# Kernel tuning notes

Measured on AMD Instinct MI355X. Metric: run time of the kernel, lower is better.

The kernel has to match this reference:

```python
import jax, jax.numpy as jnp
import numpy as np

MIN_MZ, MAX_MZ, BIN_W = 0.0, 1000.0, 0.01
NUM_BINS = int((MAX_MZ - MIN_MZ) / BIN_W)      # 100000
GROUP, OUT_PER_GROUP = 30, 3
GROUPS = NUM_BINS // GROUP                      # 3333
BINNER_OUT = GROUPS * OUT_PER_GROUP             # 9999
SCALING = 0.5
EPS = 1e-6
B, P = 256, 512                                 # pairs, padded peaks per spectrum


def setup_inputs() -> dict:
    key = jax.random.key(0)
    ks = jax.random.split(key, 10)
    # mz drawn in [0, 1100): peaks >= max_mz are dropped by the range filter (ragged-like)
    mz = jax.random.uniform(ks[0], (B, 2, P), jnp.float32, 0.0, 1100.0)
    intensities = jax.random.uniform(ks[1], (B, 2, P), jnp.float32, 1e-3, 1.0)
    s = 0.02
    return dict(
        mz=mz,
        intensities=intensities,
        binner_w=jax.random.normal(ks[2], (GROUPS, GROUP, OUT_PER_GROUP), jnp.float32) * s,
        binner_b=jax.random.normal(ks[3], (GROUPS, OUT_PER_GROUP), jnp.float32) * s,
        w0=jax.random.normal(ks[4], (BINNER_OUT, 1000), jnp.float32) * s,
        b0=jnp.zeros((1000,), jnp.float32),
        w1=jax.random.normal(ks[5], (1000, 800), jnp.float32) * s,
        b1=jnp.zeros((800,), jnp.float32),
        w2=jax.random.normal(ks[6], (800, 800), jnp.float32) * s,
        b2=jnp.zeros((800,), jnp.float32),
        we=jax.random.normal(ks[7], (800, 400), jnp.float32) * s,
        be=jnp.zeros((400,), jnp.float32),
    )


def _bin_spectra(mz, inten):
    # mz, inten: [N, P] -> binned [N, NUM_BINS] via ragged scatter-add of inten**SCALING
    mzc = jax.lax.stop_gradient(mz)             # indices are non-differentiable
    mask = (mzc >= MIN_MZ) & (mzc < MAX_MZ)
    idx = jnp.clip(((mzc - MIN_MZ) / BIN_W).astype(jnp.int32), 0, NUM_BINS - 1)
    vals = jnp.where(mask, inten ** SCALING, 0.0)
    n = mz.shape[0]
    rows = jnp.arange(n)[:, None]               # [N,1] broadcast against [N,P]
    binned = jnp.zeros((n, NUM_BINS), jnp.float32)
    return binned.at[rows, idx].add(vals)


def _encoder(binned, binner_w, binner_b, w0, b0, w1, b1, w2, b2, we, be):
    n = binned.shape[0]
    # PeakBinner: block-diagonal micro-linears over groups of 30 bins (last 10 bins unused)
    xg = binned[:, : GROUPS * GROUP].reshape(n, GROUPS, GROUP)
    x = jnp.einsum('bgi,gio->bgo', xg, binner_w) + binner_b
    x = x.reshape(n, BINNER_OUT)
    x = jax.nn.relu(x @ w0 + b0)
    x = jax.nn.relu(x @ w1 + b1)                # dropout = identity at eval
    x = jax.nn.relu(x @ w2 + b2)
    return x @ we + be                           # [N, 400]


def reference(mz, intensities, binner_w, binner_b, w0, b0, w1, b1, w2, b2, we, be):
    bp = mz.shape[0]
    n = bp * 2
    binned = _bin_spectra(mz.reshape(n, P), intensities.reshape(n, P))
    emb = _encoder(binned, binner_w, binner_b, w0, b0, w1, b1, w2, b2, we, be)
    emb = emb.reshape(bp, 2, -1)
    e1, e2 = emb[:, 0], emb[:, 1]
    n1 = jnp.maximum(jnp.linalg.norm(e1, axis=1), EPS)
    n2 = jnp.maximum(jnp.linalg.norm(e2, axis=1), EPS)
    return jnp.sum(e1 * e2, axis=1) / (n1 * n2)  # [B] cosine similarity
```

## Files before the change

### kernel.cpp

```cpp
#include <hip/hip_runtime.h>

typedef __bf16 bf16;
typedef __bf16 bf16x8 __attribute__((ext_vector_type(8)));
typedef float  f32x4  __attribute__((ext_vector_type(4)));

#define NSPEC   512
#define BOUT    9999
#define K0A     10240
#define N00     1024
#define N01     896
#define N02     896
#define N03     448

__device__ __forceinline__ void gload_lds16(const bf16* g, bf16* l) {
    auto* gp = reinterpret_cast<const __attribute__((address_space(1))) unsigned int*>(
        reinterpret_cast<uintptr_t>(g));
    auto* lp = reinterpret_cast<__attribute__((address_space(3))) unsigned int*>(
        reinterpret_cast<uintptr_t>(l));
    __builtin_amdgcn_global_load_lds(gp, lp, 16, 0, 0);
}

__device__ __forceinline__ void transpose_tile64(const float* __restrict__ src,
                                                 bf16* __restrict__ dst,
                                                 int K, int N, int K0,
                                                 float* tile, int bx, int by) {
    int n0 = bx * 64, k0 = by * 32;
    int t = threadIdx.x;
    {
        int kr = t >> 4, nc = (t & 15) * 4;
        int gk = k0 + kr;
#pragma unroll
        for (int e = 0; e < 4; ++e) {
            int gn = n0 + nc + e;
            tile[kr * 65 + nc + e] = (gk < K && gn < N) ? src[(size_t)gk * N + gn] : 0.0f;
        }
    }
    __syncthreads();
    {
        int nr = t >> 3, kc = (t & 7) * 4;
        bf16 v[4];
#pragma unroll
        for (int e = 0; e < 4; ++e) v[e] = (bf16)tile[(kc + e) * 65 + nr];
        *(ushort4*)&dst[(size_t)(n0 + nr) * K0 + k0 + kc] = *(ushort4*)v;
    }
}

__global__ __launch_bounds__(512) void prep_all(const float* __restrict__ mz,
                                                const float* __restrict__ inten,
                                                const float* __restrict__ bw,
                                                const float* __restrict__ bb,
                                                const float* __restrict__ w0,
                                                const float* __restrict__ w1,
                                                const float* __restrict__ w2,
                                                const float* __restrict__ we,
                                                bf16* __restrict__ A,
                                                bf16* __restrict__ B0t,
                                                bf16* __restrict__ B1t,
                                                bf16* __restrict__ B2t,
                                                bf16* __restrict__ BEt,
                                                float* __restrict__ psums) {
    __shared__ float smem[K0A];
    int b = blockIdx.x;
    if (b < 5120) {
        transpose_tile64(w0, B0t, BOUT, 1000, K0A, smem, b & 15, b >> 4);
    } else if (b < 5568) {
        int r = b - 5120;
        transpose_tile64(w1, B1t, 1000, 800, 1024, smem, r % 14, r / 14);
    } else if (b < 5960) {
        int r = b - 5568;
        transpose_tile64(w2, B2t, 800, 800, 896, smem, r % 14, r / 14);
    } else if (b < 6156) {
        int r = b - 5960;
        transpose_tile64(we, BEt, 800, 400, 896, smem, r % 7, r / 7);
    } else if (b < 6668) {
        const int spec = b - 6156;
        const int t = threadIdx.x;
#pragma unroll
        for (int i = 0; i < 5; ++i)
            *(float4*)&smem[(i * 512 + t) * 4] = float4{0.f, 0.f, 0.f, 0.f};
        __syncthreads();
        {
            float m = mz[(size_t)spec * 512 + t];
            float v = inten[(size_t)spec * 512 + t];
            bool mask = (m >= 0.0f) && (m < 1000.0f);
            int idx = (int)(m / 0.01f);
            idx = min(max(idx, 0), 99999);
            if (mask && idx < 99990) {
                int g = idx / 30;
                float val = sqrtf(v);
                const float* w = bw + (size_t)idx * 3;
                atomicAdd(&smem[g * 3 + 0], val * w[0]);
                atomicAdd(&smem[g * 3 + 1], val * w[1]);
                atomicAdd(&smem[g * 3 + 2], val * w[2]);
            }
        }
        __syncthreads();
        bf16* Arow = A + (size_t)spec * K0A;
#pragma unroll
        for (int i = 0; i < 5; ++i) {
            int c = (i * 512 + t) * 4;
            float4 s = *(const float4*)&smem[c];
            bf16 o[4];
            o[0] = (bf16)((c + 0 < BOUT) ? bb[c + 0] + s.x : 0.f);
            o[1] = (bf16)((c + 1 < BOUT) ? bb[c + 1] + s.y : 0.f);
            o[2] = (bf16)((c + 2 < BOUT) ? bb[c + 2] + s.z : 0.f);
            o[3] = (bf16)((c + 3 < BOUT) ? bb[c + 3] + s.w : 0.f);
            *(ushort4*)&Arow[c] = *(ushort4*)o;
        }
    } else {
        for (int i = threadIdx.x; i < 768; i += 512) psums[i] = 0.f;
    }
}

__global__ __launch_bounds__(256) void gemm0_splitk(const bf16* __restrict__ A,
                                                    const bf16* __restrict__ Bt,
                                                    float* __restrict__ Cslab) {
    constexpr int K0 = K0A, KITERS = 20, BK = 64;
    __shared__ __align__(16) bf16 As[2][64 * BK];
    __shared__ __align__(16) bf16 Bs[2][64 * BK];
    const int bid = blockIdx.x;
    const int kp = bid & 7;
    const int tile = bid >> 3;
    const int mt = tile & 7, nt = tile >> 3;
    const int tid = threadIdx.x, wave = tid >> 6, lane = tid & 63;
    const int wm = wave & 1, wn = wave >> 1;
    const int lrow = lane & 15, quad = lane >> 4;

    const bf16* Ag = A  + (size_t)(mt * 64) * K0 + kp * KITERS * BK;
    const bf16* Bg = Bt + (size_t)(nt * 64) * K0 + kp * KITERS * BK;

    auto stage = [&](int buf, int kk) {
        const int k = kk * BK;
#pragma unroll
        for (int j = 0; j < 2; ++j) {
            int row0 = j * 32 + wave * 8;
            int row = row0 + (lane >> 3);
            int ch  = (lane & 7) ^ (row & 7);
            gload_lds16(Ag + (size_t)row * K0 + k + ch * 8, &As[buf][row0 * BK]);
            gload_lds16(Bg + (size_t)row * K0 + k + ch * 8, &Bs[buf][row0 * BK]);
        }
    };

    f32x4 acc[2][2] = {};
    stage(0, 0);
    for (int kk = 0; kk < KITERS; ++kk) {
        const int cur = kk & 1;
        __syncthreads();
        if (kk + 1 < KITERS) stage(cur ^ 1, kk + 1);
#pragma unroll
        for (int ks = 0; ks < 2; ++ks) {
            bf16x8 af[2], bfr[2];
#pragma unroll
            for (int im = 0; im < 2; ++im) {
                int r = wm * 32 + im * 16 + lrow;
                int c = ks * 4 + quad;
                af[im] = *(const bf16x8*)&As[cur][r * BK + ((c ^ (r & 7)) << 3)];
            }
#pragma unroll
            for (int in = 0; in < 2; ++in) {
                int r = wn * 32 + in * 16 + lrow;
                int c = ks * 4 + quad;
                bfr[in] = *(const bf16x8*)&Bs[cur][r * BK + ((c ^ (r & 7)) << 3)];
            }
#pragma unroll
            for (int im = 0; im < 2; ++im)
#pragma unroll
                for (int in = 0; in < 2; ++in)
                    acc[im][in] = __builtin_amdgcn_mfma_f32_16x16x32_bf16(af[im], bfr[in], acc[im][in], 0, 0, 0);
        }
    }
    float* C = Cslab + (size_t)kp * (NSPEC * N00);
#pragma unroll
    for (int im = 0; im < 2; ++im) {
        int row0 = mt * 64 + wm * 32 + im * 16 + quad * 4;
#pragma unroll
        for (int in = 0; in < 2; ++in) {
            int col = nt * 64 + wn * 32 + in * 16 + lrow;
#pragma unroll
            for (int r = 0; r < 4; ++r)
                C[(size_t)(row0 + r) * N00 + col] = acc[im][in][r];
        }
    }
}

__global__ __launch_bounds__(256) void reduce_bias_relu(const float* __restrict__ Cslab,
                                                        const float* __restrict__ b0,
                                                        bf16* __restrict__ H0b) {
    int idx = blockIdx.x * 256 + threadIdx.x;
    int r = idx >> 8, c = (idx & 255) * 4;
    float4 s = {0.f, 0.f, 0.f, 0.f};
#pragma unroll
    for (int kp = 0; kp < 8; ++kp) {
        float4 v = *(const float4*)&Cslab[(size_t)kp * (NSPEC * N00) + (size_t)r * N00 + c];
        s.x += v.x; s.y += v.y; s.z += v.z; s.w += v.w;
    }
    bf16 o[4];
    o[0] = (bf16)fmaxf(s.x + ((c + 0 < 1000) ? b0[c + 0] : 0.f), 0.f);
    o[1] = (bf16)fmaxf(s.y + ((c + 1 < 1000) ? b0[c + 1] : 0.f), 0.f);
    o[2] = (bf16)fmaxf(s.z + ((c + 2 < 1000) ? b0[c + 2] : 0.f), 0.f);
    o[3] = (bf16)fmaxf(s.w + ((c + 3 < 1000) ? b0[c + 3] : 0.f), 0.f);
    *(ushort4*)&H0b[(size_t)r * N00 + c] = *(ushort4*)o;
}

__global__ __launch_bounds__(256) void gemm_small(const bf16* __restrict__ A,
                                                  const bf16* __restrict__ Bt,
                                                  const float* __restrict__ bias,
                                                  bf16* __restrict__ Ob,
                                                  int K0, int N0, int Nreal,
                                                  int kiters, int ntiles) {
    __shared__ __align__(16) bf16 As[2][32 * 128];
    __shared__ __align__(16) bf16 Bs[2][32 * 128];
    const int bid = blockIdx.x;
    const int mt = bid / ntiles, nt = bid % ntiles;
    const int tid = threadIdx.x, wave = tid >> 6, lane = tid & 63;
    const int wm = wave & 1, wn = wave >> 1;
    const int lrow = lane & 15, quad = lane >> 4;

    const bf16* Ag = A  + (size_t)(mt * 32) * K0;
    const bf16* Bg = Bt + (size_t)(nt * 32) * K0;

    auto stage = [&](int buf, int kk) {
        const int k = kk * 128;
#pragma unroll
        for (int j = wave; j < 8; j += 4) {
            int row0 = j * 4;
            int row = row0 + (lane >> 4);
            int ch  = (lane & 15) ^ (row & 15);
            gload_lds16(Ag + (size_t)row * K0 + k + ch * 8, &As[buf][row0 * 128]);
            gload_lds16(Bg + (size_t)row * K0 + k + ch * 8, &Bs[buf][row0 * 128]);
        }
    };

    f32x4 acc = {};
    stage(0, 0);
    for (int kk = 0; kk < kiters; ++kk) {
        const int cur = kk & 1;
        __syncthreads();
        if (kk + 1 < kiters) stage(cur ^ 1, kk + 1);
#pragma unroll
        for (int ks = 0; ks < 4; ++ks) {
            int ra = wm * 16 + lrow, rb = wn * 16 + lrow;
            int c = ks * 4 + quad;
            bf16x8 af  = *(const bf16x8*)&As[cur][ra * 128 + ((c ^ (ra & 15)) << 3)];
            bf16x8 bfr = *(const bf16x8*)&Bs[cur][rb * 128 + ((c ^ (rb & 15)) << 3)];
            acc = __builtin_amdgcn_mfma_f32_16x16x32_bf16(af, bfr, acc, 0, 0, 0);
        }
    }
    int row0 = mt * 32 + wm * 16 + quad * 4;
    int col  = nt * 32 + wn * 16 + lrow;
    float bv = (col < Nreal) ? bias[col] : 0.f;
#pragma unroll
    for (int r = 0; r < 4; ++r) {
        float v = fmaxf(acc[r] + bv, 0.f);
        Ob[(size_t)(row0 + r) * N0 + col] = (bf16)v;
    }
}

__global__ __launch_bounds__(256) void gemm_last(const bf16* __restrict__ A,
                                                 const bf16* __restrict__ Bt,
                                                 const float* __restrict__ bias,
                                                 float* __restrict__ psums,
                                                 int K0, int kiters, int ntiles) {
    __shared__ __align__(16) bf16 As[2][32 * 128];
    __shared__ __align__(16) bf16 Bs[2][32 * 128];
    const int bid = blockIdx.x;
    const int mt = bid / ntiles, nt = bid % ntiles;
    const int tid = threadIdx.x, wave = tid >> 6, lane = tid & 63;
    const int wm = wave & 1, wn = wave >> 1;
    const int lrow = lane & 15, quad = lane >> 4;

    const bf16* Ag = A  + (size_t)(mt * 32) * K0;
    const bf16* Bg = Bt + (size_t)(nt * 32) * K0;

    auto stage = [&](int buf, int kk) {
        const int k = kk * 128;
#pragma unroll
        for (int j = wave; j < 8; j += 4) {
            int row0 = j * 4;
            int row = row0 + (lane >> 4);
            int ch  = (lane & 15) ^ (row & 15);
            gload_lds16(Ag + (size_t)row * K0 + k + ch * 8, &As[buf][row0 * 128]);
            gload_lds16(Bg + (size_t)row * K0 + k + ch * 8, &Bs[buf][row0 * 128]);
        }
    };

    f32x4 acc = {};
    stage(0, 0);
    for (int kk = 0; kk < kiters; ++kk) {
        const int cur = kk & 1;
        __syncthreads();
        if (kk + 1 < kiters) stage(cur ^ 1, kk + 1);
#pragma unroll
        for (int ks = 0; ks < 4; ++ks) {
            int ra = wm * 16 + lrow, rb = wn * 16 + lrow;
            int c = ks * 4 + quad;
            bf16x8 af  = *(const bf16x8*)&As[cur][ra * 128 + ((c ^ (ra & 15)) << 3)];
            bf16x8 bfr = *(const bf16x8*)&Bs[cur][rb * 128 + ((c ^ (rb & 15)) << 3)];
            acc = __builtin_amdgcn_mfma_f32_16x16x32_bf16(af, bfr, acc, 0, 0, 0);
        }
    }
    int rowbase = mt * 32 + wm * 16 + quad * 4;
    int col     = nt * 32 + wn * 16 + lrow;
    bool valid  = (col < 400);
    float bv = valid ? bias[col] : 0.f;
    float v[4];
#pragma unroll
    for (int r = 0; r < 4; ++r) v[r] = valid ? (acc[r] + bv) : 0.f;
    int p0 = rowbase >> 1;
    float sums[6] = {v[0] * v[1], v[0] * v[0], v[1] * v[1],
                     v[2] * v[3], v[2] * v[2], v[3] * v[3]};
#pragma unroll
    for (int off = 1; off < 16; off <<= 1)
#pragma unroll
        for (int s = 0; s < 6; ++s) sums[s] += __shfl_xor(sums[s], off);
    if (lrow == 0) {
#pragma unroll
        for (int s = 0; s < 3; ++s) {
            atomicAdd(&psums[(p0 + 0) * 3 + s], sums[s]);
            atomicAdd(&psums[(p0 + 1) * 3 + s], sums[3 + s]);
        }
    }
}

__global__ __launch_bounds__(256) void cosine_fin(const float* __restrict__ psums,
                                                  float* __restrict__ out) {
    int t = threadIdx.x;
    float d  = psums[t * 3 + 0];
    float s1 = psums[t * 3 + 1];
    float s2 = psums[t * 3 + 2];
    float n1 = fmaxf(sqrtf(s1), 1e-6f);
    float n2 = fmaxf(sqrtf(s2), 1e-6f);
    out[t] = d / (n1 * n2);
}

extern "C" void kernel_launch(void* const* d_in, const int* in_sizes, int n_in,
                              void* d_out, int out_size, void* d_ws, size_t ws_size,
                              hipStream_t stream) {
    const float* mz    = (const float*)d_in[0];
    const float* inten = (const float*)d_in[1];
    const float* bw    = (const float*)d_in[2];
    const float* bb    = (const float*)d_in[3];
    const float* w0    = (const float*)d_in[4];
    const float* b0    = (const float*)d_in[5];
    const float* w1    = (const float*)d_in[6];
    const float* b1    = (const float*)d_in[7];
    const float* w2    = (const float*)d_in[8];
    const float* b2    = (const float*)d_in[9];
    const float* we    = (const float*)d_in[10];
    const float* be    = (const float*)d_in[11];
    float* out = (float*)d_out;

    char* ws = (char*)d_ws;
    size_t off = 0;
    auto alloc = [&](size_t bytes) { char* p = ws + off; off += (bytes + 255) & ~(size_t)255; return p; };
    bf16*  A     = (bf16*) alloc((size_t)NSPEC * K0A * 2);
    bf16*  B0t   = (bf16*) alloc((size_t)N00 * K0A * 2);
    bf16*  B1t   = (bf16*) alloc((size_t)N01 * 1024 * 2);
    bf16*  B2t   = (bf16*) alloc((size_t)N02 * 896 * 2);
    bf16*  BEt   = (bf16*) alloc((size_t)N03 * 896 * 2);
    float* Cslab = (float*)alloc((size_t)8 * NSPEC * N00 * 4);
    bf16*  H0b   = (bf16*) alloc((size_t)NSPEC * N00 * 2);
    bf16*  H1b   = (bf16*) alloc((size_t)NSPEC * N01 * 2);
    bf16*  H2b   = (bf16*) alloc((size_t)NSPEC * N02 * 2);
    float* psums = (float*)alloc(768 * 4);

    prep_all<<<6669, 512, 0, stream>>>(mz, inten, bw, bb, w0, w1, w2, we,
                                       A, B0t, B1t, B2t, BEt, psums);
    gemm0_splitk<<<1024, 256, 0, stream>>>(A, B0t, Cslab);
    reduce_bias_relu<<<512, 256, 0, stream>>>(Cslab, b0, H0b);
    gemm_small<<<448, 256, 0, stream>>>(H0b, B1t, b1, H1b, 1024, N01, 800, 8, 28);
    gemm_small<<<448, 256, 0, stream>>>(H1b, B2t, b2, H2b, 896,  N02, 800, 7, 28);
    gemm_last<<<224, 256, 0, stream>>>(H2b, BEt, be, psums, 896, 7, 14);
    cosine_fin<<<1, 256, 0, stream>>>(psums, out);
}
```

Baseline: 167.5 us.

## Double gemm0 split-K with bf16 partials and intra-block split-K tail GEMMs

The first GEMM's split-K factor goes from 8 to 16 and its partial slabs are stored in bf16 instead of fp32, so more blocks run and the slab traffic into the reduction shrinks. The three tail GEMMs become one templated 512-thread kernel with BK=256. Two wave groups each take half of every K tile and their accumulators are combined through LDS. To support this, the tail weights and activations are padded to K=1024 and the pad columns are zeroed in prep. Rounding partial sums to bf16 adds error before they are accumulated.

```diff
diff --git a/kernel.cpp b/kernel.cpp
--- a/kernel.cpp
+++ b/kernel.cpp
@@ -8,9 +8,7 @@
 #define BOUT    9999
 #define K0A     10240
 #define N00     1024
-#define N01     896
-#define N02     896
-#define N03     448
+#define KSPLIT0 16
 
 __device__ __forceinline__ void gload_lds16(const bf16* g, bf16* l) {
     auto* gp = reinterpret_cast<const __attribute__((address_space(1))) unsigned int*>(
@@ -58,6 +56,8 @@
                                                 bf16* __restrict__ B1t,
                                                 bf16* __restrict__ B2t,
                                                 bf16* __restrict__ BEt,
+                                                bf16* __restrict__ H1b,
+                                                bf16* __restrict__ H2b,
                                                 float* __restrict__ psums) {
     __shared__ float smem[K0A];
     int b = blockIdx.x;
@@ -66,14 +66,14 @@
     } else if (b < 5568) {
         int r = b - 5120;
         transpose_tile64(w1, B1t, 1000, 800, 1024, smem, r % 14, r / 14);
-    } else if (b < 5960) {
+    } else if (b < 6016) {
         int r = b - 5568;
-        transpose_tile64(w2, B2t, 800, 800, 896, smem, r % 14, r / 14);
-    } else if (b < 6156) {
-        int r = b - 5960;
-        transpose_tile64(we, BEt, 800, 400, 896, smem, r % 7, r / 7);
-    } else if (b < 6668) {
-        const int spec = b - 6156;
+        transpose_tile64(w2, B2t, 800, 800, 1024, smem, r % 14, r / 14);
+    } else if (b < 6240) {
+        int r = b - 6016;
+        transpose_tile64(we, BEt, 800, 400, 1024, smem, r % 7, r / 7);
+    } else if (b < 6752) {
+        const int spec = b - 6240;
         const int t = threadIdx.x;
 #pragma unroll
         for (int i = 0; i < 5; ++i)
@@ -107,6 +107,14 @@
             o[3] = (bf16)((c + 3 < BOUT) ? bb[c + 3] + s.w : 0.f);
             *(ushort4*)&Arow[c] = *(ushort4*)o;
         }
+    } else if (b < 6784) {
+        int idx = b - 6752;
+        bf16* H = (idx < 16) ? H1b : H2b;
+        int sub = idx & 15;
+        int t = threadIdx.x;
+        int row = sub * 32 + (t >> 4);
+        int col = 896 + (t & 15) * 8;
+        *(uint4*)&H[(size_t)row * 1024 + col] = uint4{0u, 0u, 0u, 0u};
     } else {
         for (int i = threadIdx.x; i < 768; i += 512) psums[i] = 0.f;
     }
@@ -114,20 +122,20 @@
 
 __global__ __launch_bounds__(256) void gemm0_splitk(const bf16* __restrict__ A,
                                                     const bf16* __restrict__ Bt,
-                                                    float* __restrict__ Cslab) {
-    constexpr int K0 = K0A, KITERS = 20, BK = 64;
+                                                    bf16* __restrict__ Cslab) {
+    constexpr int K0 = K0A, KITERS = 10, BK = 64;
     __shared__ __align__(16) bf16 As[2][64 * BK];
     __shared__ __align__(16) bf16 Bs[2][64 * BK];
     const int bid = blockIdx.x;
-    const int kp = bid & 7;
-    const int tile = bid >> 3;
+    const int kp = bid & 15;
+    const int tile = bid >> 4;
     const int mt = tile & 7, nt = tile >> 3;
     const int tid = threadIdx.x, wave = tid >> 6, lane = tid & 63;
     const int wm = wave & 1, wn = wave >> 1;
     const int lrow = lane & 15, quad = lane >> 4;
 
-    const bf16* Ag = A  + (size_t)(mt * 64) * K0 + kp * KITERS * BK;
-    const bf16* Bg = Bt + (size_t)(nt * 64) * K0 + kp * KITERS * BK;
+    const bf16* Ag = A  + (size_t)(mt * 64) * K0 + kp * (KITERS * BK);
+    const bf16* Bg = Bt + (size_t)(nt * 64) * K0 + kp * (KITERS * BK);
 
     auto stage = [&](int buf, int kk) {
         const int k = kk * BK;
@@ -169,7 +177,7 @@
                     acc[im][in] = __builtin_amdgcn_mfma_f32_16x16x32_bf16(af[im], bfr[in], acc[im][in], 0, 0, 0);
         }
     }
-    float* C = Cslab + (size_t)kp * (NSPEC * N00);
+    bf16* C = Cslab + (size_t)kp * (NSPEC * N00);
 #pragma unroll
     for (int im = 0; im < 2; ++im) {
         int row0 = mt * 64 + wm * 32 + im * 16 + quad * 4;
@@ -178,146 +186,111 @@
             int col = nt * 64 + wn * 32 + in * 16 + lrow;
 #pragma unroll
             for (int r = 0; r < 4; ++r)
-                C[(size_t)(row0 + r) * N00 + col] = acc[im][in][r];
-        }
-    }
-}
-
-__global__ __launch_bounds__(256) void reduce_bias_relu(const float* __restrict__ Cslab,
+                C[(size_t)(row0 + r) * N00 + col] = (bf16)acc[im][in][r];
+        }
+    }
+}
+
+__global__ __launch_bounds__(256) void reduce_bias_relu(const bf16* __restrict__ Cslab,
                                                         const float* __restrict__ b0,
                                                         bf16* __restrict__ H0b) {
     int idx = blockIdx.x * 256 + threadIdx.x;
-    int r = idx >> 8, c = (idx & 255) * 4;
-    float4 s = {0.f, 0.f, 0.f, 0.f};
-#pragma unroll
-    for (int kp = 0; kp < 8; ++kp) {
-        float4 v = *(const float4*)&Cslab[(size_t)kp * (NSPEC * N00) + (size_t)r * N00 + c];
-        s.x += v.x; s.y += v.y; s.z += v.z; s.w += v.w;
-    }
-    bf16 o[4];
-    o[0] = (bf16)fmaxf(s.x + ((c + 0 < 1000) ? b0[c + 0] : 0.f), 0.f);
-    o[1] = (bf16)fmaxf(s.y + ((c + 1 < 1000) ? b0[c + 1] : 0.f), 0.f);
-    o[2] = (bf16)fmaxf(s.z + ((c + 2 < 1000) ? b0[c + 2] : 0.f), 0.f);
-    o[3] = (bf16)fmaxf(s.w + ((c + 3 < 1000) ? b0[c + 3] : 0.f), 0.f);
-    *(ushort4*)&H0b[(size_t)r * N00 + c] = *(ushort4*)o;
-}
-
-__global__ __launch_bounds__(256) void gemm_small(const bf16* __restrict__ A,
-                                                  const bf16* __restrict__ Bt,
-                                                  const float* __restrict__ bias,
-                                                  bf16* __restrict__ Ob,
-                                                  int K0, int N0, int Nreal,
-                                                  int kiters, int ntiles) {
-    __shared__ __align__(16) bf16 As[2][32 * 128];
-    __shared__ __align__(16) bf16 Bs[2][32 * 128];
+    int r = idx >> 7, c = (idx & 127) * 8;
+    float s[8] = {};
+#pragma unroll
+    for (int kp = 0; kp < KSPLIT0; ++kp) {
+        bf16x8 v = *(const bf16x8*)&Cslab[(size_t)kp * (NSPEC * N00) + (size_t)r * N00 + c];
+#pragma unroll
+        for (int j = 0; j < 8; ++j) s[j] += (float)v[j];
+    }
+    bf16 o[8];
+#pragma unroll
+    for (int j = 0; j < 8; ++j)
+        o[j] = (bf16)fmaxf(s[j] + ((c + j < 1000) ? b0[c + j] : 0.f), 0.f);
+    *(uint4*)&H0b[(size_t)r * N00 + c] = *(uint4*)o;
+}
+
+template <bool LAST>
+__global__ __launch_bounds__(512) void gemm_tail(const bf16* __restrict__ A,
+                                                 const bf16* __restrict__ Bt,
+                                                 const float* __restrict__ bias,
+                                                 bf16* __restrict__ Ob,
+                                                 float* __restrict__ psums,
+                                                 int Nreal, int ntiles) {
+    constexpr int BK = 256, KITERS = 4;
+    __shared__ __align__(16) bf16 As[2][32 * BK];
+    __shared__ __align__(16) bf16 Bs[2][32 * BK];
+    __shared__ f32x4 xacc[4][64];
     const int bid = blockIdx.x;
     const int mt = bid / ntiles, nt = bid % ntiles;
     const int tid = threadIdx.x, wave = tid >> 6, lane = tid & 63;
-    const int wm = wave & 1, wn = wave >> 1;
+    const int g = wave >> 2, w2 = wave & 3;
+    const int wm = w2 & 1, wn = w2 >> 1;
     const int lrow = lane & 15, quad = lane >> 4;
 
-    const bf16* Ag = A  + (size_t)(mt * 32) * K0;
-    const bf16* Bg = Bt + (size_t)(nt * 32) * K0;
+    const bf16* Ag = A  + (size_t)(mt * 32) * 1024;
+    const bf16* Bg = Bt + (size_t)(nt * 32) * 1024;
 
     auto stage = [&](int buf, int kk) {
-        const int k = kk * 128;
-#pragma unroll
-        for (int j = wave; j < 8; j += 4) {
-            int row0 = j * 4;
-            int row = row0 + (lane >> 4);
-            int ch  = (lane & 15) ^ (row & 15);
-            gload_lds16(Ag + (size_t)row * K0 + k + ch * 8, &As[buf][row0 * 128]);
-            gload_lds16(Bg + (size_t)row * K0 + k + ch * 8, &Bs[buf][row0 * 128]);
+        const int k = kk * BK;
+#pragma unroll
+        for (int j = 0; j < 2; ++j) {
+            int row0 = (wave + j * 8) * 2;
+            int row = row0 + (lane >> 5);
+            int ch  = (lane & 31) ^ (row & 31);
+            gload_lds16(Ag + (size_t)row * 1024 + k + ch * 8, &As[buf][row0 * BK]);
+            gload_lds16(Bg + (size_t)row * 1024 + k + ch * 8, &Bs[buf][row0 * BK]);
         }
     };
 
     f32x4 acc = {};
     stage(0, 0);
-    for (int kk = 0; kk < kiters; ++kk) {
+    for (int kk = 0; kk < KITERS; ++kk) {
         const int cur = kk & 1;
         __syncthreads();
-        if (kk + 1 < kiters) stage(cur ^ 1, kk + 1);
+        if (kk + 1 < KITERS) stage(cur ^ 1, kk + 1);
 #pragma unroll
         for (int ks = 0; ks < 4; ++ks) {
             int ra = wm * 16 + lrow, rb = wn * 16 + lrow;
-            int c = ks * 4 + quad;
-            bf16x8 af  = *(const bf16x8*)&As[cur][ra * 128 + ((c ^ (ra & 15)) << 3)];
-            bf16x8 bfr = *(const bf16x8*)&Bs[cur][rb * 128 + ((c ^ (rb & 15)) << 3)];
+            int c = g * 16 + ks * 4 + quad;
+            bf16x8 af  = *(const bf16x8*)&As[cur][ra * BK + ((c ^ (ra & 31)) << 3)];
+            bf16x8 bfr = *(const bf16x8*)&Bs[cur][rb * BK + ((c ^ (rb & 31)) << 3)];
             acc = __builtin_amdgcn_mfma_f32_16x16x32_bf16(af, bfr, acc, 0, 0, 0);
         }
     }
-    int row0 = mt * 32 + wm * 16 + quad * 4;
-    int col  = nt * 32 + wn * 16 + lrow;
-    float bv = (col < Nreal) ? bias[col] : 0.f;
-#pragma unroll
-    for (int r = 0; r < 4; ++r) {
-        float v = fmaxf(acc[r] + bv, 0.f);
-        Ob[(size_t)(row0 + r) * N0 + col] = (bf16)v;
-    }
-}
-
-__global__ __launch_bounds__(256) void gemm_last(const bf16* __restrict__ A,
-                                                 const bf16* __restrict__ Bt,
-                                                 const float* __restrict__ bias,
-                                                 float* __restrict__ psums,
-                                                 int K0, int kiters, int ntiles) {
-    __shared__ __align__(16) bf16 As[2][32 * 128];
-    __shared__ __align__(16) bf16 Bs[2][32 * 128];
-    const int bid = blockIdx.x;
-    const int mt = bid / ntiles, nt = bid % ntiles;
-    const int tid = threadIdx.x, wave = tid >> 6, lane = tid & 63;
-    const int wm = wave & 1, wn = wave >> 1;
-    const int lrow = lane & 15, quad = lane >> 4;
-
-    const bf16* Ag = A  + (size_t)(mt * 32) * K0;
-    const bf16* Bg = Bt + (size_t)(nt * 32) * K0;
-
-    auto stage = [&](int buf, int kk) {
-        const int k = kk * 128;
-#pragma unroll
-        for (int j = wave; j < 8; j += 4) {
-            int row0 = j * 4;
-            int row = row0 + (lane >> 4);
-            int ch  = (lane & 15) ^ (row & 15);
-            gload_lds16(Ag + (size_t)row * K0 + k + ch * 8, &As[buf][row0 * 128]);
-            gload_lds16(Bg + (size_t)row * K0 + k + ch * 8, &Bs[buf][row0 * 128]);
-        }
-    };
-
-    f32x4 acc = {};
-    stage(0, 0);
-    for (int kk = 0; kk < kiters; ++kk) {
-        const int cur = kk & 1;
-        __syncthreads();
-        if (kk + 1 < kiters) stage(cur ^ 1, kk + 1);
-#pragma unroll
-        for (int ks = 0; ks < 4; ++ks) {
-            int ra = wm * 16 + lrow, rb = wn * 16 + lrow;
-            int c = ks * 4 + quad;
-            bf16x8 af  = *(const bf16x8*)&As[cur][ra * 128 + ((c ^ (ra & 15)) << 3)];
-            bf16x8 bfr = *(const bf16x8*)&Bs[cur][rb * 128 + ((c ^ (rb & 15)) << 3)];
-            acc = __builtin_amdgcn_mfma_f32_16x16x32_bf16(af, bfr, acc, 0, 0, 0);
-        }
-    }
-    int rowbase = mt * 32 + wm * 16 + quad * 4;
-    int col     = nt * 32 + wn * 16 + lrow;
-    bool valid  = (col < 400);
-    float bv = valid ? bias[col] : 0.f;
-    float v[4];
-#pragma unroll
-    for (int r = 0; r < 4; ++r) v[r] = valid ? (acc[r] + bv) : 0.f;
-    int p0 = rowbase >> 1;
-    float sums[6] = {v[0] * v[1], v[0] * v[0], v[1] * v[1],
-                     v[2] * v[3], v[2] * v[2], v[3] * v[3]};
-#pragma unroll
-    for (int off = 1; off < 16; off <<= 1)
-#pragma unroll
-        for (int s = 0; s < 6; ++s) sums[s] += __shfl_xor(sums[s], off);
-    if (lrow == 0) {
-#pragma unroll
-        for (int s = 0; s < 3; ++s) {
-            atomicAdd(&psums[(p0 + 0) * 3 + s], sums[s]);
-            atomicAdd(&psums[(p0 + 1) * 3 + s], sums[3 + s]);
+    __syncthreads();
+    if (g == 1) xacc[w2][lane] = acc;
+    __syncthreads();
+    if (g == 0) {
+        f32x4 o = xacc[w2][lane];
+        acc[0] += o[0]; acc[1] += o[1]; acc[2] += o[2]; acc[3] += o[3];
+        int row0 = mt * 32 + wm * 16 + quad * 4;
+        int col  = nt * 32 + wn * 16 + lrow;
+        if (!LAST) {
+            float bv = (col < Nreal) ? bias[col] : 0.f;
+#pragma unroll
+            for (int r = 0; r < 4; ++r)
+                Ob[(size_t)(row0 + r) * 1024 + col] = (bf16)fmaxf(acc[r] + bv, 0.f);
+        } else {
+            bool valid = (col < 400);
+            float bv = valid ? bias[col] : 0.f;
+            float v[4];
+#pragma unroll
+            for (int r = 0; r < 4; ++r) v[r] = valid ? (acc[r] + bv) : 0.f;
+            int p0 = row0 >> 1;
+            float sums[6] = {v[0] * v[1], v[0] * v[0], v[1] * v[1],
+                             v[2] * v[3], v[2] * v[2], v[3] * v[3]};
+#pragma unroll
+            for (int off = 1; off < 16; off <<= 1)
+#pragma unroll
+                for (int s = 0; s < 6; ++s) sums[s] += __shfl_xor(sums[s], off);
+            if (lrow == 0) {
+#pragma unroll
+                for (int s = 0; s < 3; ++s) {
+                    atomicAdd(&psums[(p0 + 0) * 3 + s], sums[s]);
+                    atomicAdd(&psums[(p0 + 1) * 3 + s], sums[3 + s]);
+                }
+            }
         }
     }
 }
@@ -355,21 +328,21 @@
     auto alloc = [&](size_t bytes) { char* p = ws + off; off += (bytes + 255) & ~(size_t)255; return p; };
     bf16*  A     = (bf16*) alloc((size_t)NSPEC * K0A * 2);
     bf16*  B0t   = (bf16*) alloc((size_t)N00 * K0A * 2);
-    bf16*  B1t   = (bf16*) alloc((size_t)N01 * 1024 * 2);
-    bf16*  B2t   = (bf16*) alloc((size_t)N02 * 896 * 2);
-    bf16*  BEt   = (bf16*) alloc((size_t)N03 * 896 * 2);
-    float* Cslab = (float*)alloc((size_t)8 * NSPEC * N00 * 4);
-    bf16*  H0b   = (bf16*) alloc((size_t)NSPEC * N00 * 2);
-    bf16*  H1b   = (bf16*) alloc((size_t)NSPEC * N01 * 2);
-    bf16*  H2b   = (bf16*) alloc((size_t)NSPEC * N02 * 2);
+    bf16*  B1t   = (bf16*) alloc((size_t)896 * 1024 * 2);
+    bf16*  B2t   = (bf16*) alloc((size_t)896 * 1024 * 2);
+    bf16*  BEt   = (bf16*) alloc((size_t)448 * 1024 * 2);
+    bf16*  Cslab = (bf16*) alloc((size_t)KSPLIT0 * NSPEC * N00 * 2);
+    bf16*  H0b   = (bf16*) alloc((size_t)NSPEC * 1024 * 2);
+    bf16*  H1b   = (bf16*) alloc((size_t)NSPEC * 1024 * 2);
+    bf16*  H2b   = (bf16*) alloc((size_t)NSPEC * 1024 * 2);
     float* psums = (float*)alloc(768 * 4);
 
-    prep_all<<<6669, 512, 0, stream>>>(mz, inten, bw, bb, w0, w1, w2, we,
-                                       A, B0t, B1t, B2t, BEt, psums);
-    gemm0_splitk<<<1024, 256, 0, stream>>>(A, B0t, Cslab);
-    reduce_bias_relu<<<512, 256, 0, stream>>>(Cslab, b0, H0b);
-    gemm_small<<<448, 256, 0, stream>>>(H0b, B1t, b1, H1b, 1024, N01, 800, 8, 28);
-    gemm_small<<<448, 256, 0, stream>>>(H1b, B2t, b2, H2b, 896,  N02, 800, 7, 28);
-    gemm_last<<<224, 256, 0, stream>>>(H2b, BEt, be, psums, 896, 7, 14);
+    prep_all<<<6785, 512, 0, stream>>>(mz, inten, bw, bb, w0, w1, w2, we,
+                                       A, B0t, B1t, B2t, BEt, H1b, H2b, psums);
+    gemm0_splitk<<<2048, 256, 0, stream>>>(A, B0t, Cslab);
+    reduce_bias_relu<<<256, 256, 0, stream>>>(Cslab, b0, H0b);
+    gemm_tail<false><<<448, 512, 0, stream>>>(H0b, B1t, b1, H1b, nullptr, 800, 28);
+    gemm_tail<false><<<448, 512, 0, stream>>>(H1b, B2t, b2, H2b, nullptr, 800, 28);
+    gemm_tail<true ><<<224, 512, 0, stream>>>(H2b, BEt, be, nullptr, psums, 400, 14);
     cosine_fin<<<1, 256, 0, stream>>>(psums, out);
 }
```

Measured after the change: 168.2 us. No clear change (+0.4%).
